# Kernel optimization log

Hardware: AMD Instinct MI355X
Metric: run time of the kernel (lower is better)

Reference implementation:

```python
import jax, jax.numpy as jnp
import numpy as np

NEG_INF = 100000.0  # matches torch INF tensor in source


def setup_inputs() -> dict:
    key = jax.random.key(0)
    ks = jax.random.split(key, 8)
    B, S, D = 4, 4096, 256
    query = jax.random.normal(ks[0], (B, S, D), dtype=jnp.float32)
    k_in = jax.random.normal(ks[1], (B, S, D), dtype=jnp.float32)
    value = jax.random.normal(ks[2], (B, S, D), dtype=jnp.float32)
    mask = jax.random.randint(ks[3], (B, S), 0, 2).astype(bool)
    # nn.Linear(dim, dim) params: weight [out, in], bias [out]
    lim = 1.0 / np.sqrt(D)
    Wq = jax.random.uniform(ks[4], (D, D), jnp.float32, -lim, lim)
    bq = jax.random.uniform(ks[5], (D,), jnp.float32, -lim, lim)
    Wk = jax.random.uniform(ks[6], (D, D), jnp.float32, -lim, lim)
    bk = jax.random.uniform(ks[7], (D,), jnp.float32, -lim, lim)
    return {"query": query, "key": k_in, "value": value, "mask": mask,
            "Wq": Wq, "bq": bq, "Wk": Wk, "bk": bk}


def reference(query, key, value, mask, Wq, bq, Wk, bk):
    D = query.shape[-1]
    q = jnp.einsum('bsd,ed->bse', query, Wq) + bq  # query_proj
    k = jnp.einsum('bsd,ed->bse', key, Wk) + bk    # key_proj
    score = jnp.einsum('bqd,bkd->bqk', q, k) / jnp.sqrt(jnp.float32(D))
    # mask (B,S) broadcast over last dim: masks whole query rows where mask is False
    score = jnp.where(mask[:, :, None], score, -NEG_INF)
    attn = jax.nn.softmax(score, axis=-1)  # [B, S, S]
    context = jnp.einsum('bqk,bkd->bqd', attn, value)
    return (context, attn)
```

## Files before the change

kernel.cpp:

```cpp
#include <hip/hip_runtime.h>

typedef __attribute__((ext_vector_type(8))) _Float16 f16x8;
typedef __attribute__((ext_vector_type(4))) _Float16 f16x4;
typedef __attribute__((ext_vector_type(4))) float f32x4;
typedef _Float16 half_t;

#define MFMA32(a, b, c) __builtin_amdgcn_mfma_f32_16x16x32_f16((a), (b), (c), 0, 0, 0)
#define MFMA16(a, b, c) __builtin_amdgcn_mfma_f32_16x16x16f16((a), (b), (c), 0, 0, 0)

__device__ __forceinline__ void gload_lds16(const half_t* g, half_t* l) {
    __builtin_amdgcn_global_load_lds(
        (const __attribute__((address_space(1))) unsigned int*)g,
        (__attribute__((address_space(3))) unsigned int*)l, 16, 0, 0);
}


__global__ __launch_bounds__(512, 2)
void proj_kernel(const float* __restrict__ X, const float* __restrict__ W,
                 const float* __restrict__ bias, half_t* __restrict__ out)
{
    __shared__ half_t Wl[256 * 264];
    int tid = threadIdx.x;
    for (int i = 0; i < 128; ++i) {
        int idx = tid + i * 512;
        int r = idx >> 8, c = idx & 255;
        Wl[r * 264 + c] = (half_t)W[idx];
    }
    __syncthreads();

    int w = tid >> 6, lane = tid & 63, l15 = lane & 15, hi = lane >> 4;
    int row0 = blockIdx.x * 128 + w * 16;

    const float* xb = X + (size_t)(row0 + l15) * 256 + hi * 8;
    f32x4 acc[16];
#pragma unroll
    for (int n = 0; n < 16; ++n) acc[n] = (f32x4){0.f, 0.f, 0.f, 0.f};

#pragma unroll
    for (int kd = 0; kd < 8; ++kd) {
        const float4* xv = (const float4*)(xb + kd * 32);
        float4 x0 = xv[0], x1 = xv[1];
        f16x8 a = { (half_t)x0.x, (half_t)x0.y, (half_t)x0.z, (half_t)x0.w,
                    (half_t)x1.x, (half_t)x1.y, (half_t)x1.z, (half_t)x1.w };
#pragma unroll
        for (int n = 0; n < 16; ++n) {
            f16x8 bf = *(const f16x8*)&Wl[(n * 16 + l15) * 264 + kd * 32 + hi * 8];
            acc[n] = MFMA32(a, bf, acc[n]);
        }
    }

#pragma unroll
    for (int n = 0; n < 16; ++n) {
        float bv = bias[n * 16 + l15];
#pragma unroll
        for (int r = 0; r < 4; ++r) {
            float v = acc[n][r] + bv;
            out[(size_t)(row0 + 4 * hi + r) * 256 + n * 16 + l15] = (half_t)v;
        }
    }
}

__global__ __launch_bounds__(256)
void vt_kernel(const float* __restrict__ V, half_t* __restrict__ vt)
{
    __shared__ half_t tile[64][65];
    int tid = threadIdx.x;
    int b = blockIdx.x >> 8, rest = blockIdx.x & 255;
    int s0 = (rest >> 2) * 64, d0 = (rest & 3) * 64;
#pragma unroll
    for (int i = 0; i < 16; ++i) {
        int srow = i * 4 + (tid >> 6);
        int dcol = tid & 63;
        tile[srow][dcol] = (half_t)V[(size_t)(b * 4096 + s0 + srow) * 256 + d0 + dcol];
    }
    __syncthreads();
#pragma unroll
    for (int i = 0; i < 16; ++i) {
        int drow = i * 4 + (tid >> 6);
        int scol = tid & 63;
        vt[(size_t)(b * 256 + d0 + drow) * 4096 + s0 + scol] = tile[scol][drow];
    }
}

__global__ __launch_bounds__(1024, 4)
void attn_kernel(const half_t* __restrict__ qh, const half_t* __restrict__ kg_,
                 const half_t* __restrict__ vt, const int* __restrict__ mask,
                 float* __restrict__ ctx_out, float* __restrict__ attn_out)
{
    __shared__ __align__(16) char pool[131072 + 1024];
    half_t* Klds = (half_t*)pool;
    half_t* Vlds = (half_t*)(pool + 65536);
    float*  redsum = (float*)(pool + 131072);

    const int tid = threadIdx.x;
    const int w = tid >> 6, lane = tid & 63, l15 = lane & 15, hi = lane >> 4;
    const int qg = w >> 2, khs = w & 3;
    const int bid = blockIdx.x;
    const int wgid = (bid & 7) * 32 + (bid >> 3);
    const int b = wgid >> 6, q0 = (wgid & 63) * 64;
    const int q = q0 + qg * 16 + l15;

    const half_t* kg = kg_ + (size_t)b * 4096 * 256;
    const half_t* vg = vt + (size_t)b * 256 * 4096;

    const bool km = mask[b * 4096 + q] != 0;

    f16x8 qf[8];
    const half_t* qb = qh + (size_t)(b * 4096 + q) * 256 + hi * 8;
#pragma unroll
    for (int kd = 0; kd < 8; ++kd) qf[kd] = *(const f16x8*)(qb + kd * 32);

    auto stageK = [&](int t, int buf) {
#pragma unroll
        for (int i = 0; i < 2; ++i) {
            int row = w * 4 + i * 2 + (lane >> 5);
            int u = lane & 31;
            const half_t* src = kg + (size_t)(t * 64 + row) * 256 + (u ^ (row & 7)) * 8;
            gload_lds16(src, Klds + buf * 16384 + (w * 4 + i * 2) * 256);
        }
    };
    auto stageV = [&](int t, int buf) {
#pragma unroll
        for (int i = 0; i < 2; ++i) {
            int d = w * 16 + i * 8 + (lane >> 3);
            int u = lane & 7;
            const half_t* src = vg + (size_t)d * 4096 + t * 64 + (u ^ (d & 7)) * 8;
            gload_lds16(src, Vlds + buf * 16384 + (w * 16 + i * 8) * 64);
        }
    };

    const int arow = khs * 16 + l15;
    const int asw = arow & 7;

    stageK(0, 0);
    __syncthreads();
    float vsum = 0.f;
    for (int t = 0; t < 64; ++t) {
        if (t < 63) stageK(t + 1, (t + 1) & 1);
        const half_t* ab = Klds + (t & 1) * 16384 + arow * 256;
        f32x4 c = {0.f, 0.f, 0.f, 0.f};
#pragma unroll
        for (int kd = 0; kd < 8; ++kd) {
            f16x8 A = *(const f16x8*)(ab + ((kd * 4 + hi) ^ asw) * 8);
            c = MFMA32(A, qf[kd], c);
        }
#pragma unroll
        for (int r = 0; r < 4; ++r)
            vsum += __expf(km ? c[r] * 0.0625f : 0.0f);
        __syncthreads();
    }
    vsum += __shfl_xor(vsum, 16, 64);
    vsum += __shfl_xor(vsum, 32, 64);
    if (lane < 16) redsum[(qg * 4 + khs) * 16 + l15] = vsum;
    __syncthreads();
    const float inv = 1.0f / (redsum[(qg * 4 + 0) * 16 + l15] +
                              redsum[(qg * 4 + 1) * 16 + l15] +
                              redsum[(qg * 4 + 2) * 16 + l15] +
                              redsum[(qg * 4 + 3) * 16 + l15]);

    f32x4 acc[16];
#pragma unroll
    for (int n = 0; n < 16; ++n) acc[n] = (f32x4){0.f, 0.f, 0.f, 0.f};

    stageK(0, 0); stageV(0, 0);
    __syncthreads();

    float* aout = attn_out + (size_t)(b * 4096 + q) * 4096 + khs * 16 + 4 * hi;

    for (int t = 0; t < 64; ++t) {
        if (t < 63) { stageK(t + 1, (t + 1) & 1); stageV(t + 1, (t + 1) & 1); }

        const half_t* ab = Klds + (t & 1) * 16384 + arow * 256;
        f32x4 c = {0.f, 0.f, 0.f, 0.f};
#pragma unroll
        for (int kd = 0; kd < 8; ++kd) {
            f16x8 A = *(const f16x8*)(ab + ((kd * 4 + hi) ^ asw) * 8);
            c = MFMA32(A, qf[kd], c);
        }
        f32x4 a;
#pragma unroll
        for (int r = 0; r < 4; ++r)
            a[r] = __expf(km ? c[r] * 0.0625f : 0.0f) * inv;
        __builtin_nontemporal_store(a, (f32x4*)(aout + t * 64));

        f16x4 p = { (half_t)a[0], (half_t)a[1], (half_t)a[2], (half_t)a[3] };

        const half_t* vb = Vlds + (t & 1) * 16384;
#pragma unroll
        for (int n = 0; n < 16; ++n) {
            int d = n * 16 + l15;
            f16x4 Bv = *(const f16x4*)(vb + d * 64 + (((khs * 32 + hi * 8) ^ ((d & 7) << 4)) >> 1));
            acc[n] = MFMA16(p, Bv, acc[n]);
        }
        __syncthreads();
    }

    float* rc = (float*)pool + qg * (16 * 256);
    for (int rnd = 0; rnd < 4; ++rnd) {
        if (khs == rnd) {
#pragma unroll
            for (int n = 0; n < 16; ++n)
#pragma unroll
                for (int r = 0; r < 4; ++r) {
                    int idx = (4 * hi + r) * 256 + n * 16 + l15;
                    if (rnd == 0) rc[idx] = acc[n][r];
                    else          rc[idx] += acc[n][r];
                }
        }
        __syncthreads();
    }

    float* cbase = ctx_out + (size_t)(b * 4096 + q0) * 256;
    for (int e = tid * 4; e < 64 * 256; e += 1024 * 4)
        *(f32x4*)(cbase + e) = *(const f32x4*)((const float*)pool + e);
}

extern "C" void kernel_launch(void* const* d_in, const int* in_sizes, int n_in,
                              void* d_out, int out_size, void* d_ws, size_t ws_size,
                              hipStream_t stream) {
    const float* query = (const float*)d_in[0];
    const float* key   = (const float*)d_in[1];
    const float* value = (const float*)d_in[2];
    const int*   mask  = (const int*)d_in[3];
    const float* Wq    = (const float*)d_in[4];
    const float* bq    = (const float*)d_in[5];
    const float* Wk    = (const float*)d_in[6];
    const float* bk    = (const float*)d_in[7];

    float* ctx  = (float*)d_out;
    float* attn = ctx + (size_t)4 * 4096 * 256;

    half_t* qh = (half_t*)d_ws;
    half_t* kh = qh + (size_t)4 * 4096 * 256;
    half_t* vt = kh + (size_t)4 * 4096 * 256;

    proj_kernel<<<128, 512, 0, stream>>>(query, Wq, bq, qh);
    proj_kernel<<<128, 512, 0, stream>>>(key,   Wk, bk, kh);
    vt_kernel<<<1024, 256, 0, stream>>>(value, vt);
    attn_kernel<<<256, 1024, 0, stream>>>(qh, kh, vt, mask, ctx, attn);
}
```

Before: 247.8 us.

## Split key range across blocks with separate row-sum and context-reduce kernels

The single attention kernel is split into a row-sum kernel and a main attention kernel. Each block now covers 128 queries and half of the key range, and the two halves' softmax denominators are combined through a small workspace buffer. The partial contexts are folded with an extra reduce kernel, and the attn store switches from nontemporal to a regular store. This is meant to give each block more query rows per K/V tile for better reuse, at the cost of two extra launches and an extra read/write pass over ctx.

After: 310.4 us. +25.3%, slower.

```diff
diff --git a/kernel.cpp b/kernel.cpp
--- a/kernel.cpp
+++ b/kernel.cpp
@@ -83,26 +83,22 @@
 }
 
 __global__ __launch_bounds__(1024, 4)
-void attn_kernel(const half_t* __restrict__ qh, const half_t* __restrict__ kg_,
-                 const half_t* __restrict__ vt, const int* __restrict__ mask,
-                 float* __restrict__ ctx_out, float* __restrict__ attn_out)
-{
-    __shared__ __align__(16) char pool[131072 + 1024];
+void sum_kernel(const half_t* __restrict__ qh, const half_t* __restrict__ kg_,
+                const int* __restrict__ mask, float* __restrict__ sums)
+{
+    __shared__ __align__(16) char pool[65536 + 1024];
     half_t* Klds = (half_t*)pool;
-    half_t* Vlds = (half_t*)(pool + 65536);
-    float*  redsum = (float*)(pool + 131072);
+    float* redsum = (float*)(pool + 65536);
 
     const int tid = threadIdx.x;
     const int w = tid >> 6, lane = tid & 63, l15 = lane & 15, hi = lane >> 4;
-    const int qg = w >> 2, khs = w & 3;
+    const int qsub = w >> 1, kh = w & 1;
     const int bid = blockIdx.x;
     const int wgid = (bid & 7) * 32 + (bid >> 3);
-    const int b = wgid >> 6, q0 = (wgid & 63) * 64;
-    const int q = q0 + qg * 16 + l15;
-
-    const half_t* kg = kg_ + (size_t)b * 4096 * 256;
-    const half_t* vg = vt + (size_t)b * 256 * 4096;
-
+    const int b = wgid >> 6, kbh = (wgid >> 5) & 1, qt = wgid & 31;
+    const int q = qt * 128 + qsub * 16 + l15;
+
+    const half_t* kg = kg_ + (size_t)b * 4096 * 256 + (size_t)kbh * 2048 * 256;
     const bool km = mask[b * 4096 + q] != 0;
 
     f16x8 qf[8];
@@ -119,6 +115,76 @@
             gload_lds16(src, Klds + buf * 16384 + (w * 4 + i * 2) * 256);
         }
     };
+
+    stageK(0, 0);
+    __syncthreads();
+    float vsum = 0.f;
+    for (int t = 0; t < 32; ++t) {
+        if (t < 31) stageK(t + 1, (t + 1) & 1);
+        const half_t* kb = Klds + (t & 1) * 16384;
+#pragma unroll
+        for (int s = 0; s < 2; ++s) {
+            const int arow = kh * 32 + s * 16 + l15, asw = arow & 7;
+            const half_t* ab = kb + arow * 256;
+            f32x4 c = {0.f, 0.f, 0.f, 0.f};
+#pragma unroll
+            for (int kd = 0; kd < 8; ++kd) {
+                f16x8 A = *(const f16x8*)(ab + ((kd * 4 + hi) ^ asw) * 8);
+                c = MFMA32(A, qf[kd], c);
+            }
+#pragma unroll
+            for (int r = 0; r < 4; ++r)
+                vsum += __expf(km ? c[r] * 0.0625f : 0.0f);
+        }
+        __syncthreads();
+    }
+    vsum += __shfl_xor(vsum, 16, 64);
+    vsum += __shfl_xor(vsum, 32, 64);
+    if (lane < 16) redsum[(qsub * 2 + kh) * 16 + l15] = vsum;
+    __syncthreads();
+    if (kh == 0 && lane < 16)
+        sums[(size_t)kbh * 16384 + b * 4096 + q] =
+            redsum[(qsub * 2 + 0) * 16 + l15] + redsum[(qsub * 2 + 1) * 16 + l15];
+}
+
+__global__ __launch_bounds__(1024, 4)
+void attn_kernel(const half_t* __restrict__ qh, const half_t* __restrict__ kg_,
+                 const half_t* __restrict__ vt, const int* __restrict__ mask,
+                 const float* __restrict__ sums,
+                 float* __restrict__ ctx_out, float* __restrict__ attn_out,
+                 float* __restrict__ wsp)
+{
+    __shared__ __align__(16) char pool[131072];
+    half_t* Klds = (half_t*)pool;
+    half_t* Vlds = (half_t*)(pool + 65536);
+
+    const int tid = threadIdx.x;
+    const int w = tid >> 6, lane = tid & 63, l15 = lane & 15, hi = lane >> 4;
+    const int qsub = w >> 1, kh = w & 1;
+    const int bid = blockIdx.x;
+    const int wgid = (bid & 7) * 32 + (bid >> 3);
+    const int b = wgid >> 6, kbh = (wgid >> 5) & 1, qt = wgid & 31;
+    const int q = qt * 128 + qsub * 16 + l15;
+
+    const half_t* kg = kg_ + (size_t)b * 4096 * 256 + (size_t)kbh * 2048 * 256;
+    const half_t* vg = vt + (size_t)b * 256 * 4096 + kbh * 2048;
+    const bool km = mask[b * 4096 + q] != 0;
+    const float inv = 1.0f / (sums[b * 4096 + q] + sums[16384 + b * 4096 + q]);
+
+    f16x8 qf[8];
+    const half_t* qb = qh + (size_t)(b * 4096 + q) * 256 + hi * 8;
+#pragma unroll
+    for (int kd = 0; kd < 8; ++kd) qf[kd] = *(const f16x8*)(qb + kd * 32);
+
+    auto stageK = [&](int t, int buf) {
+#pragma unroll
+        for (int i = 0; i < 2; ++i) {
+            int row = w * 4 + i * 2 + (lane >> 5);
+            int u = lane & 31;
+            const half_t* src = kg + (size_t)(t * 64 + row) * 256 + (u ^ (row & 7)) * 8;
+            gload_lds16(src, Klds + buf * 16384 + (w * 4 + i * 2) * 256);
+        }
+    };
     auto stageV = [&](int t, int buf) {
 #pragma unroll
         for (int i = 0; i < 2; ++i) {
@@ -129,90 +195,83 @@
         }
     };
 
-    const int arow = khs * 16 + l15;
-    const int asw = arow & 7;
-
-    stageK(0, 0);
-    __syncthreads();
-    float vsum = 0.f;
-    for (int t = 0; t < 64; ++t) {
-        if (t < 63) stageK(t + 1, (t + 1) & 1);
-        const half_t* ab = Klds + (t & 1) * 16384 + arow * 256;
-        f32x4 c = {0.f, 0.f, 0.f, 0.f};
-#pragma unroll
-        for (int kd = 0; kd < 8; ++kd) {
-            f16x8 A = *(const f16x8*)(ab + ((kd * 4 + hi) ^ asw) * 8);
-            c = MFMA32(A, qf[kd], c);
-        }
-#pragma unroll
-        for (int r = 0; r < 4; ++r)
-            vsum += __expf(km ? c[r] * 0.0625f : 0.0f);
+    f32x4 acc[16];
+#pragma unroll
+    for (int n = 0; n < 16; ++n) acc[n] = (f32x4){0.f, 0.f, 0.f, 0.f};
+
+    stageK(0, 0); stageV(0, 0);
+    __syncthreads();
+
+    float* aout = attn_out + (size_t)(b * 4096 + q) * 4096 + kbh * 2048 + kh * 32;
+
+    for (int t = 0; t < 32; ++t) {
+        if (t < 31) { stageK(t + 1, (t + 1) & 1); stageV(t + 1, (t + 1) & 1); }
+
+        const half_t* kb = Klds + (t & 1) * 16384;
+        const char* vb = (const char*)(Vlds + (t & 1) * 16384);
+#pragma unroll
+        for (int s = 0; s < 2; ++s) {
+            const int arow = kh * 32 + s * 16 + l15, asw = arow & 7;
+            const half_t* ab = kb + arow * 256;
+            f32x4 c = {0.f, 0.f, 0.f, 0.f};
+#pragma unroll
+            for (int kd = 0; kd < 8; ++kd) {
+                f16x8 A = *(const f16x8*)(ab + ((kd * 4 + hi) ^ asw) * 8);
+                c = MFMA32(A, qf[kd], c);
+            }
+            f32x4 a;
+#pragma unroll
+            for (int r = 0; r < 4; ++r)
+                a[r] = __expf(km ? c[r] * 0.0625f : 0.0f) * inv;
+            *(f32x4*)(aout + t * 64 + s * 16 + 4 * hi) = a;
+
+            f16x4 p = { (half_t)a[0], (half_t)a[1], (half_t)a[2], (half_t)a[3] };
+            const int koffB = kh * 64 + s * 32 + hi * 8;
+#pragma unroll
+            for (int n = 0; n < 16; ++n) {
+                int d = n * 16 + l15;
+                f16x4 Bv = *(const f16x4*)(vb + d * 128 + (koffB ^ ((d & 7) << 4)));
+                acc[n] = MFMA16(p, Bv, acc[n]);
+            }
+        }
         __syncthreads();
     }
-    vsum += __shfl_xor(vsum, 16, 64);
-    vsum += __shfl_xor(vsum, 32, 64);
-    if (lane < 16) redsum[(qg * 4 + khs) * 16 + l15] = vsum;
-    __syncthreads();
-    const float inv = 1.0f / (redsum[(qg * 4 + 0) * 16 + l15] +
-                              redsum[(qg * 4 + 1) * 16 + l15] +
-                              redsum[(qg * 4 + 2) * 16 + l15] +
-                              redsum[(qg * 4 + 3) * 16 + l15]);
-
-    f32x4 acc[16];
-#pragma unroll
-    for (int n = 0; n < 16; ++n) acc[n] = (f32x4){0.f, 0.f, 0.f, 0.f};
-
-    stageK(0, 0); stageV(0, 0);
-    __syncthreads();
-
-    float* aout = attn_out + (size_t)(b * 4096 + q) * 4096 + khs * 16 + 4 * hi;
-
-    for (int t = 0; t < 64; ++t) {
-        if (t < 63) { stageK(t + 1, (t + 1) & 1); stageV(t + 1, (t + 1) & 1); }
-
-        const half_t* ab = Klds + (t & 1) * 16384 + arow * 256;
-        f32x4 c = {0.f, 0.f, 0.f, 0.f};
-#pragma unroll
-        for (int kd = 0; kd < 8; ++kd) {
-            f16x8 A = *(const f16x8*)(ab + ((kd * 4 + hi) ^ asw) * 8);
-            c = MFMA32(A, qf[kd], c);
-        }
-        f32x4 a;
-#pragma unroll
-        for (int r = 0; r < 4; ++r)
-            a[r] = __expf(km ? c[r] * 0.0625f : 0.0f) * inv;
-        __builtin_nontemporal_store(a, (f32x4*)(aout + t * 64));
-
-        f16x4 p = { (half_t)a[0], (half_t)a[1], (half_t)a[2], (half_t)a[3] };
-
-        const half_t* vb = Vlds + (t & 1) * 16384;
-#pragma unroll
-        for (int n = 0; n < 16; ++n) {
-            int d = n * 16 + l15;
-            f16x4 Bv = *(const f16x4*)(vb + d * 64 + (((khs * 32 + hi * 8) ^ ((d & 7) << 4)) >> 1));
-            acc[n] = MFMA16(p, Bv, acc[n]);
-        }
-        __syncthreads();
-    }
-
-    float* rc = (float*)pool + qg * (16 * 256);
-    for (int rnd = 0; rnd < 4; ++rnd) {
-        if (khs == rnd) {
-#pragma unroll
-            for (int n = 0; n < 16; ++n)
-#pragma unroll
-                for (int r = 0; r < 4; ++r) {
-                    int idx = (4 * hi + r) * 256 + n * 16 + l15;
-                    if (rnd == 0) rc[idx] = acc[n][r];
-                    else          rc[idx] += acc[n][r];
-                }
-        }
-        __syncthreads();
-    }
-
-    float* cbase = ctx_out + (size_t)(b * 4096 + q0) * 256;
-    for (int e = tid * 4; e < 64 * 256; e += 1024 * 4)
-        *(f32x4*)(cbase + e) = *(const f32x4*)((const float*)pool + e);
+
+    float* fold = (float*)pool;
+    if (kh == 1) {
+        float* F = fold + qsub * 4096;
+#pragma unroll
+        for (int n = 0; n < 16; ++n)
+#pragma unroll
+            for (int r = 0; r < 4; ++r)
+                F[(4 * hi + r) * 256 + n * 16 + l15] = acc[n][r];
+    }
+    __syncthreads();
+    if (kh == 0) {
+        float* F = fold + qsub * 4096;
+#pragma unroll
+        for (int n = 0; n < 16; ++n)
+#pragma unroll
+            for (int r = 0; r < 4; ++r)
+                F[(4 * hi + r) * 256 + n * 16 + l15] += acc[n][r];
+    }
+    __syncthreads();
+
+    float* dst = (kbh == 0 ? ctx_out : wsp) + (size_t)(b * 4096 + qt * 128) * 256;
+    for (int e = tid * 4; e < 128 * 256; e += 1024 * 4)
+        *(f32x4*)(dst + e) = *(const f32x4*)(fold + e);
+}
+
+__global__ __launch_bounds__(256)
+void reduce_kernel(float* __restrict__ ctx, const float* __restrict__ wsp)
+{
+    const size_t total = (size_t)4 * 4096 * 256;
+    size_t stride = (size_t)gridDim.x * 256 * 4;
+    for (size_t i = ((size_t)blockIdx.x * 256 + threadIdx.x) * 4; i < total; i += stride) {
+        f32x4 a = *(const f32x4*)(ctx + i);
+        f32x4 bb = *(const f32x4*)(wsp + i);
+        *(f32x4*)(ctx + i) = a + bb;
+    }
 }
 
 extern "C" void kernel_launch(void* const* d_in, const int* in_sizes, int n_in,
@@ -230,12 +289,17 @@
     float* ctx  = (float*)d_out;
     float* attn = ctx + (size_t)4 * 4096 * 256;
 
-    half_t* qh = (half_t*)d_ws;
-    half_t* kh = qh + (size_t)4 * 4096 * 256;
-    half_t* vt = kh + (size_t)4 * 4096 * 256;
+    const size_t MB = 1024 * 1024;
+    half_t* qh   = (half_t*)d_ws;
+    half_t* khw  = (half_t*)((char*)d_ws + 8 * MB);
+    half_t* vt   = (half_t*)((char*)d_ws + 16 * MB);
+    float*  sums = (float*)((char*)d_ws + 24 * MB);
+    float*  wsp  = (float*)((char*)d_ws + 24 * MB + 131072);
 
     proj_kernel<<<128, 512, 0, stream>>>(query, Wq, bq, qh);
-    proj_kernel<<<128, 512, 0, stream>>>(key,   Wk, bk, kh);
+    proj_kernel<<<128, 512, 0, stream>>>(key,   Wk, bk, khw);
     vt_kernel<<<1024, 256, 0, stream>>>(value, vt);
-    attn_kernel<<<256, 1024, 0, stream>>>(qh, kh, vt, mask, ctx, attn);
-}
+    sum_kernel<<<256, 1024, 0, stream>>>(qh, khw, mask, sums);
+    attn_kernel<<<256, 1024, 0, stream>>>(qh, khw, vt, mask, sums, ctx, attn, wsp);
+    reduce_kernel<<<1024, 256, 0, stream>>>(ctx, wsp);
+}
```
